# Optimization experiments

Measured on AMD Instinct MI355X. Metric: run time of the kernel, lower is better.

The kernel has to match this reference:

```python
import jax, jax.numpy as jnp
import numpy as np
import math

B, D, NH, HD, FF, P, IMG = 4, 768, 12, 64, 3072, 16, 256
L = (IMG // P) ** 2      # 256 tokens
PD = P * P * 3           # 768 patch dim
GRID = IMG // P          # 16


def setup_inputs() -> dict:
    key = jax.random.key(0)
    ks = iter(jax.random.split(key, 80))
    def nrm(shape, s=0.02):
        return jax.random.normal(next(ks), shape, jnp.float32) * s
    return {
        "x": jax.random.normal(next(ks), (B, 3, IMG, IMG), jnp.float32),
        "pe_norm_w": jnp.ones((PD,), jnp.float32),
        "pe_proj_w": nrm((PD, D)),
        "pe_proj_b": jnp.zeros((D,), jnp.float32),
        "pe_norm_out_w": jnp.ones((D,), jnp.float32),
        "pos_embed": nrm((1, L, D)),
        "in_attn_norm_w": jnp.ones((6, D), jnp.float32),
        "in_qkv_w": nrm((6, D, 3 * D)),
        "in_out_w": nrm((6, D, D)),
        "in_ff_norm_w": jnp.ones((6, D), jnp.float32),
        "in_w1": nrm((6, D, 2 * FF)),
        "in_w2": nrm((6, FF, D)),
        "mid_attn_norm_w": jnp.ones((3, D), jnp.float32),
        "mid_qkv_w": nrm((3, D, 3 * D)),
        "mid_out_w": nrm((3, D, D)),
        "mid_ff_norm_w": jnp.ones((3, D), jnp.float32),
        "mid_w1": nrm((3, D, 2 * FF)),
        "mid_w2": nrm((3, FF, D)),
        "out_skip_w": nrm((2 * D, D)),
        "out_skip_b": jnp.zeros((D,), jnp.float32),
        "out_attn_norm_w": jnp.ones((D,), jnp.float32),
        "out_qkv_w": nrm((D, 3 * D)),
        "out_out_w": nrm((D, D)),
        "out_ff_norm_w": jnp.ones((D,), jnp.float32),
        "out_w1": nrm((D, 2 * FF)),
        "out_w2": nrm((FF, D)),
        "final_norm_w": jnp.ones((D,), jnp.float32),
        "ol_proj_w": nrm((D, PD)),
        "ol_proj_b": jnp.zeros((PD,), jnp.float32),
        "rb_conv_in_w": nrm((128, 3, 3, 3), 0.1),
        "rb_gn_w": jnp.ones((5, 128), jnp.float32),
        "rb_gn_b": jnp.zeros((5, 128), jnp.float32),
        "rb_conv1_w": nrm((128, 1, 5, 5), 0.1),
        "rb_conv2_w": nrm((128, 1, 5, 5), 0.1),
        "head_conv_w": nrm((1, 128, 3, 3), 0.1),
    }


def _mish(x):
    return x * jnp.tanh(jax.nn.softplus(x))


def _rms(x, w, eps=1e-5):
    return x * jax.lax.rsqrt(jnp.mean(x * x, axis=-1, keepdims=True) + eps) * w


def _attn(x, qkv_w, out_w):
    b, l, _ = x.shape
    q, k, v = jnp.split(x @ qkv_w, 3, axis=-1)
    s = 1.0 / math.sqrt(HD)  # applied to BOTH q and k, as in source
    q = (q * s).reshape(b, l, NH, HD)
    k = (k * s).reshape(b, l, NH, HD)
    v = v.reshape(b, l, NH, HD)
    logits = jnp.einsum('bqhd,bkhd->bhqk', q, k).astype(jnp.float32)
    w = jax.nn.softmax(logits, axis=-1).astype(x.dtype)
    o = jnp.einsum('bhqk,bkhd->bqhd', w, v).reshape(b, l, NH * HD)
    return o @ out_w


def _ff(x, w1, w2):
    a, g = jnp.split(x @ w1, 2, axis=-1)
    return (_mish(a) * g) @ w2


def _block(x, an, qkv, ow, fn, w1, w2):
    x = x + _attn(_rms(x, an), qkv, ow)
    x = x + _ff(_rms(x, fn), w1, w2)
    return x


def _gn(x, w, b, groups=8, eps=1e-5):
    bb, c, h, ww = x.shape
    xg = x.reshape(bb, groups, c // groups, h, ww)
    m = jnp.mean(xg, axis=(2, 3, 4), keepdims=True)
    v = jnp.var(xg, axis=(2, 3, 4), keepdims=True)
    xn = ((xg - m) * jax.lax.rsqrt(v + eps)).reshape(bb, c, h, ww)
    return xn * w[:, None, None] + b[:, None, None]


def _conv(x, w, pad, dil=1, groups=1):
    xp = jnp.pad(x, ((0, 0), (0, 0), (pad, pad), (pad, pad)), mode='reflect')
    return jax.lax.conv_general_dilated(
        xp, w, window_strides=(1, 1), padding='VALID', rhs_dilation=(dil, dil),
        feature_group_count=groups, dimension_numbers=('NCHW', 'OIHW', 'NCHW'))


def _forward(x, pe_norm_w, pe_proj_w, pe_proj_b, pe_norm_out_w, pos_embed,
             in_attn_norm_w, in_qkv_w, in_out_w, in_ff_norm_w, in_w1, in_w2,
             mid_attn_norm_w, mid_qkv_w, mid_out_w, mid_ff_norm_w, mid_w1, mid_w2,
             out_skip_w, out_skip_b, out_attn_norm_w, out_qkv_w, out_out_w,
             out_ff_norm_w, out_w1, out_w2, final_norm_w, ol_proj_w, ol_proj_b,
             rb_conv_in_w, rb_gn_w, rb_gn_b, rb_conv1_w, rb_conv2_w, head_conv_w):
    b = x.shape[0]
    # PatchEmbed: b c (h p1) (w p2) -> b (h w) (p1 p2 c)
    t = x.reshape(b, 3, GRID, P, GRID, P).transpose(0, 2, 4, 3, 5, 1).reshape(b, L, PD)
    t = _rms(t, pe_norm_w)
    t = t @ pe_proj_w + pe_proj_b
    t = _rms(t, pe_norm_out_w)
    t = t + pos_embed
    # U-ViT trunk: 6 in blocks (skips saved), 3 middle, 1 out block (source typo -> single out block)
    skips = []
    for i in range(6):
        t = _block(t, in_attn_norm_w[i], in_qkv_w[i], in_out_w[i],
                   in_ff_norm_w[i], in_w1[i], in_w2[i])
        skips.append(t)
    for i in range(3):
        t = _block(t, mid_attn_norm_w[i], mid_qkv_w[i], mid_out_w[i],
                   mid_ff_norm_w[i], mid_w1[i], mid_w2[i])
    t = jnp.concatenate([t, skips[-1]], axis=-1) @ out_skip_w + out_skip_b
    t = _block(t, out_attn_norm_w, out_qkv_w, out_out_w, out_ff_norm_w, out_w1, out_w2)
    t = _rms(t, final_norm_w)
    # OutBlock: proj, dropout(eval=identity), unpatchify to b 3 256 256
    t = t @ ol_proj_w + ol_proj_b
    img = t.reshape(b, GRID, GRID, P, P, 3).transpose(0, 5, 1, 3, 2, 4).reshape(b, 3, IMG, IMG)
    # ResNetBlock(128)
    h = _conv(img, rb_conv_in_w, 1)
    h = _mish(_gn(h, rb_gn_w[0], rb_gn_b[0]))
    res = h
    h = _mish(_gn(_conv(h, rb_conv1_w, 2, 1, 128), rb_gn_w[1], rb_gn_b[1]))
    h = res + h
    h = _mish(_gn(h, rb_gn_w[2], rb_gn_b[2]))
    res = h
    h = _mish(_gn(_conv(h, rb_conv2_w, 6, 3, 128), rb_gn_w[3], rb_gn_b[3]))
    h = res + h
    h = _mish(_gn(h, rb_gn_w[4], rb_gn_b[4]))
    return _conv(h, head_conv_w, 1)  # [B, 1, 256, 256]


def reference(x, pe_norm_w, pe_proj_w, pe_proj_b, pe_norm_out_w, pos_embed,
              in_attn_norm_w, in_qkv_w, in_out_w, in_ff_norm_w, in_w1, in_w2,
              mid_attn_norm_w, mid_qkv_w, mid_out_w, mid_ff_norm_w, mid_w1, mid_w2,
              out_skip_w, out_skip_b, out_attn_norm_w, out_qkv_w, out_out_w,
              out_ff_norm_w, out_w1, out_w2, final_norm_w, ol_proj_w, ol_proj_b,
              rb_conv_in_w, rb_gn_w, rb_gn_b, rb_conv1_w, rb_conv2_w, head_conv_w):
    return _forward(x, pe_norm_w, pe_proj_w, pe_proj_b, pe_norm_out_w, pos_embed,
                    in_attn_norm_w, in_qkv_w, in_out_w, in_ff_norm_w, in_w1, in_w2,
                    mid_attn_norm_w, mid_qkv_w, mid_out_w, mid_ff_norm_w, mid_w1, mid_w2,
                    out_skip_w, out_skip_b, out_attn_norm_w, out_qkv_w, out_out_w,
                    out_ff_norm_w, out_w1, out_w2, final_norm_w, ol_proj_w, ol_proj_b,
                    rb_conv_in_w, rb_gn_w, rb_gn_b, rb_conv1_w, rb_conv2_w, head_conv_w)
```

## Files before the change

### kernel.cpp

```cpp
#include <hip/hip_runtime.h>
#include <math.h>

#define B_ 4
#define D_ 768
#define NH_ 12
#define HD_ 64
#define FF_ 3072
#define L_ 256
#define PD_ 768
#define GRID_ 16
#define P_ 16
#define IMG_ 256
#define M_ (B_*L_)
#define NCONV_ (B_*128*IMG_*IMG_)

typedef __attribute__((ext_vector_type(8))) short short8;
typedef __attribute__((ext_vector_type(4))) float f32x4;
typedef __attribute__((ext_vector_type(4))) unsigned short us4;
typedef __attribute__((ext_vector_type(8))) unsigned short us8;
typedef unsigned short ushort_t;

__device__ __forceinline__ float mishf(float x){
    float e = __expf(x);
    float u = (1.f + e) * (1.f + e);
    return x * (1.f - 2.f / (u + 1.f));
}

__device__ __forceinline__ int refl(int i, int n){
    if (i < 0) i = -i;
    if (i >= n) i = 2*n - 2 - i;
    return i;
}

__device__ __forceinline__ ushort_t f2bf(float f){
    unsigned int u = __float_as_uint(f);
    unsigned int r = (u + 0x7FFFu + ((u >> 16) & 1u)) >> 16;
    return (ushort_t)r;
}
__device__ __forceinline__ float bf2f(ushort_t u){
    return __uint_as_float(((unsigned int)u) << 16);
}

__device__ __forceinline__ void block_red2(float& s, float& q){
    #pragma unroll
    for (int o = 32; o > 0; o >>= 1){ s += __shfl_down(s, o); q += __shfl_down(q, o); }
    __shared__ float r1[4], r2[4];
    int tid = threadIdx.x;
    if ((tid & 63) == 0){ r1[tid>>6] = s; r2[tid>>6] = q; }
    __syncthreads();
    if (tid == 0){ s = r1[0]+r1[1]+r1[2]+r1[3]; q = r2[0]+r2[1]+r2[2]+r2[3]; }
    __syncthreads();
}

__global__ __launch_bounds__(256) void k_patchify(const float* __restrict__ x, float* __restrict__ t){
    int idx = blockIdx.x*256 + threadIdx.x;
    int d = idx % PD_; int l = (idx/PD_) % L_; int b = idx/(PD_*L_);
    int c = d % 3; int p = d / 3; int p1 = p / P_; int p2 = p % P_;
    int gh = l / GRID_; int gw = l % GRID_;
    int sy = gh*P_ + p1, sx = gw*P_ + p2;
    t[idx] = x[(((size_t)b*3 + c)*IMG_ + sy)*IMG_ + sx];
}

__global__ __launch_bounds__(256) void k_wt(const float* __restrict__ b0, const float* __restrict__ b1,
                                            const float* __restrict__ b2, int n0, int n1,
                                            ushort_t* __restrict__ dst, int K, int N){
    int z = blockIdx.z;
    size_t sz = (size_t)K * N;
    const float* src = (z < n0) ? b0 + (size_t)z*sz
                     : (z < n0+n1) ? b1 + (size_t)(z-n0)*sz
                     : b2 + (size_t)(z-n0-n1)*sz;
    ushort_t* out = dst + (size_t)z*sz;
    __shared__ float ld[32][33];
    int k0 = blockIdx.y*32, nc0 = blockIdx.x*32;
    int tid = threadIdx.x;
    int c = tid & 31, r8 = tid >> 5;
    #pragma unroll
    for (int i = 0; i < 4; ++i){
        int k = r8 + i*8;
        ld[k][c] = src[(size_t)(k0+k)*N + nc0 + c];
    }
    __syncthreads();
    #pragma unroll
    for (int i = 0; i < 4; ++i){
        int n = r8 + i*8;
        out[(size_t)(nc0+n)*K + k0 + c] = f2bf(ld[c][n]);
    }
}

template<bool OUT_BF>
__global__ __launch_bounds__(256) void k_rms(const float* __restrict__ x, const float* __restrict__ w,
                                             const float* __restrict__ addv, void* __restrict__ yv){
    int row = blockIdx.x;
    const float* xr = x + (size_t)row * D_;
    float s = 0.f;
    for (int i = threadIdx.x; i < D_; i += 256){ float v = xr[i]; s += v*v; }
    __shared__ float red[256];
    red[threadIdx.x] = s; __syncthreads();
    for (int o = 128; o > 0; o >>= 1){
        if (threadIdx.x < o) red[threadIdx.x] += red[threadIdx.x+o];
        __syncthreads();
    }
    float rstd = rsqrtf(red[0]/(float)D_ + 1e-5f);
    int l = row % L_;
    for (int i = threadIdx.x; i < D_; i += 256){
        float v = xr[i]*rstd*w[i];
        if (addv) v += addv[(size_t)l*D_ + i];
        if (OUT_BF) ((ushort_t*)yv)[(size_t)row*D_ + i] = f2bf(v);
        else        ((float*)yv)[(size_t)row*D_ + i] = v;
    }
}

template<bool OBF, int SPLITK>
__global__ __launch_bounds__(256) void k_gemm(const ushort_t* __restrict__ A, const ushort_t* __restrict__ Wt,
                                              void* __restrict__ Cv, const float* __restrict__ bias,
                                              const float* __restrict__ res, int N, int K){
    __shared__ ushort_t As[2][64][40];
    __shared__ ushort_t Ws[2][64][40];
    int tid = threadIdx.x;
    int lane = tid & 63, wid = tid >> 6;
    int wr = wid >> 1, wc = wid & 1;
    int row0 = blockIdx.y * 64, col0 = blockIdx.x * 64;
    f32x4 acc[2][2];
    #pragma unroll
    for (int i = 0; i < 2; ++i)
        #pragma unroll
        for (int j = 0; j < 2; ++j) acc[i][j] = (f32x4){0.f,0.f,0.f,0.f};

    int lg = lane >> 4, lr = lane & 15;
    int sr = tid >> 2, sk = (tid & 3) * 8;
    int kc = K / SPLITK;
    int k0 = (SPLITK > 1) ? blockIdx.z * kc : 0;
    const ushort_t* arow = A  + (size_t)(row0 + sr)*K + k0 + sk;
    const ushort_t* wrow = Wt + (size_t)(col0 + sr)*K + k0 + sk;

    for (int kt = 0; kt < kc; kt += 64){
        __syncthreads();
        *(short8*)&As[0][sr][sk] = *(const short8*)(arow + kt);
        *(short8*)&As[1][sr][sk] = *(const short8*)(arow + kt + 32);
        *(short8*)&Ws[0][sr][sk] = *(const short8*)(wrow + kt);
        *(short8*)&Ws[1][sr][sk] = *(const short8*)(wrow + kt + 32);
        __syncthreads();
        short8 a0[2], a1[2], b0[2], b1[2];
        #pragma unroll
        for (int i = 0; i < 2; ++i){
            a0[i] = *(const short8*)(&As[0][wr*32 + i*16 + lr][lg*8]);
            a1[i] = *(const short8*)(&As[1][wr*32 + i*16 + lr][lg*8]);
        }
        #pragma unroll
        for (int j = 0; j < 2; ++j){
            b0[j] = *(const short8*)(&Ws[0][wc*32 + j*16 + lr][lg*8]);
            b1[j] = *(const short8*)(&Ws[1][wc*32 + j*16 + lr][lg*8]);
        }
        #pragma unroll
        for (int i = 0; i < 2; ++i)
            #pragma unroll
            for (int j = 0; j < 2; ++j){
                acc[i][j] = __builtin_amdgcn_mfma_f32_16x16x32_bf16(a0[i], b0[j], acc[i][j], 0, 0, 0);
                acc[i][j] = __builtin_amdgcn_mfma_f32_16x16x32_bf16(a1[i], b1[j], acc[i][j], 0, 0, 0);
            }
    }
    if (SPLITK > 1){
        float* Pp = (float*)Cv + (size_t)blockIdx.z * M_ * N;
        #pragma unroll
        for (int i = 0; i < 2; ++i)
            #pragma unroll
            for (int j = 0; j < 2; ++j)
                #pragma unroll
                for (int q = 0; q < 4; ++q){
                    int m = row0 + wr*32 + i*16 + lg*4 + q;
                    int n = col0 + wc*32 + j*16 + lr;
                    Pp[(size_t)m*N + n] = acc[i][j][q];
                }
    } else {
        #pragma unroll
        for (int i = 0; i < 2; ++i)
            #pragma unroll
            for (int j = 0; j < 2; ++j)
                #pragma unroll
                for (int q = 0; q < 4; ++q){
                    int m = row0 + wr*32 + i*16 + lg*4 + q;
                    int n = col0 + wc*32 + j*16 + lr;
                    float v = acc[i][j][q];
                    if (bias) v += bias[n];
                    size_t o = (size_t)m*N + n;
                    if (OBF){
                        ((ushort_t*)Cv)[o] = f2bf(v);
                    } else {
                        if (res) v += res[o];
                        ((float*)Cv)[o] = v;
                    }
                }
    }
}

__global__ __launch_bounds__(256) void k_skred(const float* __restrict__ Pp, float* __restrict__ t){
    int idx = blockIdx.x*256 + threadIdx.x;
    size_t e = (size_t)idx*4;
    f32x4 s = *(const f32x4*)(t + e);
    #pragma unroll
    for (int z = 0; z < 4; ++z){
        f32x4 v = *(const f32x4*)(Pp + (size_t)z*M_*D_ + e);
        s.x += v.x; s.y += v.y; s.z += v.z; s.w += v.w;
    }
    *(f32x4*)(t + e) = s;
}

__global__ __launch_bounds__(256) void k_gemm_glu(const ushort_t* __restrict__ A, const ushort_t* __restrict__ Wt,
                                                  ushort_t* __restrict__ Cb, int K){
    __shared__ ushort_t As[2][64][40];
    __shared__ ushort_t Wa[2][64][40];
    __shared__ ushort_t Wg[2][64][40];
    int tid = threadIdx.x;
    int lane = tid & 63, wid = tid >> 6;
    int wr = wid >> 1, wc = wid & 1;
    int row0 = blockIdx.y * 64, col0 = blockIdx.x * 64;
    f32x4 aa[2][2], ag[2][2];
    #pragma unroll
    for (int i = 0; i < 2; ++i)
        #pragma unroll
        for (int j = 0; j < 2; ++j){ aa[i][j] = (f32x4){0.f,0.f,0.f,0.f}; ag[i][j] = (f32x4){0.f,0.f,0.f,0.f}; }

    int lg = lane >> 4, lr = lane & 15;
    int sr = tid >> 2, sk = (tid & 3) * 8;
    const ushort_t* arow = A + (size_t)(row0+sr)*K + sk;
    const ushort_t* war = Wt + (size_t)(col0+sr)*K + sk;
    const ushort_t* wgr = Wt + (size_t)(FF_+col0+sr)*K + sk;

    for (int kt = 0; kt < K; kt += 64){
        __syncthreads();
        *(short8*)&As[0][sr][sk] = *(const short8*)(arow + kt);
        *(short8*)&As[1][sr][sk] = *(const short8*)(arow + kt + 32);
        *(short8*)&Wa[0][sr][sk] = *(const short8*)(war + kt);
        *(short8*)&Wa[1][sr][sk] = *(const short8*)(war + kt + 32);
        *(short8*)&Wg[0][sr][sk] = *(const short8*)(wgr + kt);
        *(short8*)&Wg[1][sr][sk] = *(const short8*)(wgr + kt + 32);
        __syncthreads();
        short8 a0[2], a1[2], ba0[2], ba1[2], bg0[2], bg1[2];
        #pragma unroll
        for (int i = 0; i < 2; ++i){
            a0[i] = *(const short8*)(&As[0][wr*32 + i*16 + lr][lg*8]);
            a1[i] = *(const short8*)(&As[1][wr*32 + i*16 + lr][lg*8]);
        }
        #pragma unroll
        for (int j = 0; j < 2; ++j){
            ba0[j] = *(const short8*)(&Wa[0][wc*32 + j*16 + lr][lg*8]);
            ba1[j] = *(const short8*)(&Wa[1][wc*32 + j*16 + lr][lg*8]);
            bg0[j] = *(const short8*)(&Wg[0][wc*32 + j*16 + lr][lg*8]);
            bg1[j] = *(const short8*)(&Wg[1][wc*32 + j*16 + lr][lg*8]);
        }
        #pragma unroll
        for (int i = 0; i < 2; ++i)
            #pragma unroll
            for (int j = 0; j < 2; ++j){
                aa[i][j] = __builtin_amdgcn_mfma_f32_16x16x32_bf16(a0[i], ba0[j], aa[i][j], 0, 0, 0);
                aa[i][j] = __builtin_amdgcn_mfma_f32_16x16x32_bf16(a1[i], ba1[j], aa[i][j], 0, 0, 0);
                ag[i][j] = __builtin_amdgcn_mfma_f32_16x16x32_bf16(a0[i], bg0[j], ag[i][j], 0, 0, 0);
                ag[i][j] = __builtin_amdgcn_mfma_f32_16x16x32_bf16(a1[i], bg1[j], ag[i][j], 0, 0, 0);
            }
    }
    #pragma unroll
    for (int i = 0; i < 2; ++i)
        #pragma unroll
        for (int j = 0; j < 2; ++j)
            #pragma unroll
            for (int q = 0; q < 4; ++q){
                int m = row0 + wr*32 + i*16 + lg*4 + q;
                int n = col0 + wc*32 + j*16 + lr;
                Cb[(size_t)m*FF_ + n] = f2bf(mishf(aa[i][j][q]) * ag[i][j][q]);
            }
}

__global__ __launch_bounds__(256) void k_attn(const ushort_t* __restrict__ qkv, ushort_t* __restrict__ out){
    int qt = blockIdx.x, h = blockIdx.y, b = blockIdx.z;
    const ushort_t* base = qkv + (size_t)b * L_ * 3 * D_;
    __shared__ ushort_t Qs[64][72];
    __shared__ ushort_t KVs[64][72];
    __shared__ ushort_t Ps[64][268];
    __shared__ float red[8][64];
    int tid = threadIdx.x;
    int lane = tid & 63, w = tid >> 6;
    int lr = lane & 15, lg = lane >> 4;

    {
        int r = tid >> 2, c = (tid & 3) * 16;
        const ushort_t* src = base + (size_t)(qt*64 + r)*3*D_ + h*HD_ + c;
        *(us8*)&Qs[r][c]   = *(const us8*)src;
        *(us8*)&Qs[r][c+8] = *(const us8*)(src + 8);
    }

    f32x4 sacc[4][4];
    #pragma unroll
    for (int kt = 0; kt < 4; ++kt)
        #pragma unroll
        for (int mi = 0; mi < 4; ++mi) sacc[kt][mi] = (f32x4){0.f,0.f,0.f,0.f};

    for (int kt = 0; kt < 4; ++kt){
        __syncthreads();
        {
            int r = tid >> 2, c = (tid & 3) * 16;
            const ushort_t* src = base + (size_t)(kt*64 + r)*3*D_ + D_ + h*HD_ + c;
            *(us8*)&KVs[r][c]   = *(const us8*)src;
            *(us8*)&KVs[r][c+8] = *(const us8*)(src + 8);
        }
        __syncthreads();
        short8 bk0 = *(const short8*)&KVs[w*16 + lr][lg*8];
        short8 bk1 = *(const short8*)&KVs[w*16 + lr][32 + lg*8];
        #pragma unroll
        for (int mi = 0; mi < 4; ++mi){
            short8 a0 = *(const short8*)&Qs[mi*16 + lr][lg*8];
            short8 a1 = *(const short8*)&Qs[mi*16 + lr][32 + lg*8];
            sacc[kt][mi] = __builtin_amdgcn_mfma_f32_16x16x32_bf16(a0, bk0, sacc[kt][mi], 0, 0, 0);
            sacc[kt][mi] = __builtin_amdgcn_mfma_f32_16x16x32_bf16(a1, bk1, sacc[kt][mi], 0, 0, 0);
        }
    }

    const float inv64 = 1.0f/64.0f;
    float gm[4][4], linv[4][4];
    #pragma unroll
    for (int mi = 0; mi < 4; ++mi){
        #pragma unroll
        for (int r = 0; r < 4; ++r){
            float v = fmaxf(fmaxf(sacc[0][mi][r], sacc[1][mi][r]), fmaxf(sacc[2][mi][r], sacc[3][mi][r]));
            v = fmaxf(v, __shfl_xor(v, 1));
            v = fmaxf(v, __shfl_xor(v, 2));
            v = fmaxf(v, __shfl_xor(v, 4));
            v = fmaxf(v, __shfl_xor(v, 8));
            gm[mi][r] = v;
            if (lr == 0) red[w][mi*16 + lg*4 + r] = v;
        }
    }
    __syncthreads();
    #pragma unroll
    for (int mi = 0; mi < 4; ++mi){
        #pragma unroll
        for (int r = 0; r < 4; ++r){
            int row = mi*16 + lg*4 + r;
            float m = fmaxf(fmaxf(red[0][row], red[1][row]), fmaxf(red[2][row], red[3][row]));
            gm[mi][r] = m;
            float sum = 0.f;
            #pragma unroll
            for (int kt = 0; kt < 4; ++kt){
                float p = __expf((sacc[kt][mi][r] - m) * inv64);
                Ps[row][kt*64 + w*16 + lr] = f2bf(p);
                sum += p;
            }
            sum += __shfl_xor(sum, 1);
            sum += __shfl_xor(sum, 2);
            sum += __shfl_xor(sum, 4);
            sum += __shfl_xor(sum, 8);
            linv[mi][r] = sum;
            if (lr == 0) red[4 + w][row] = sum;
        }
    }
    __syncthreads();
    #pragma unroll
    for (int mi = 0; mi < 4; ++mi){
        #pragma unroll
        for (int r = 0; r < 4; ++r){
            int row = mi*16 + lg*4 + r;
            linv[mi][r] = 1.0f / (red[4][row] + red[5][row] + red[6][row] + red[7][row]);
        }
    }

    f32x4 oacc[4];
    #pragma unroll
    for (int mi = 0; mi < 4; ++mi) oacc[mi] = (f32x4){0.f,0.f,0.f,0.f};
    for (int kt = 0; kt < 4; ++kt){
        __syncthreads();
        {
            int k = tid & 63, dg = tid >> 6;
            const ushort_t* src = base + (size_t)(kt*64 + k)*3*D_ + 2*D_ + h*HD_ + dg*16;
            us8 v0 = *(const us8*)src;
            us8 v1 = *(const us8*)(src + 8);
            #pragma unroll
            for (int j = 0; j < 8; ++j) KVs[dg*16 + j][k] = v0[j];
            #pragma unroll
            for (int j = 0; j < 8; ++j) KVs[dg*16 + 8 + j][k] = v1[j];
        }
        __syncthreads();
        short8 bv0 = *(const short8*)&KVs[w*16 + lr][lg*8];
        short8 bv1 = *(const short8*)&KVs[w*16 + lr][32 + lg*8];
        #pragma unroll
        for (int mi = 0; mi < 4; ++mi){
            short8 a0 = *(const short8*)&Ps[mi*16 + lr][kt*64 + lg*8];
            short8 a1 = *(const short8*)&Ps[mi*16 + lr][kt*64 + 32 + lg*8];
            oacc[mi] = __builtin_amdgcn_mfma_f32_16x16x32_bf16(a0, bv0, oacc[mi], 0, 0, 0);
            oacc[mi] = __builtin_amdgcn_mfma_f32_16x16x32_bf16(a1, bv1, oacc[mi], 0, 0, 0);
        }
    }
    #pragma unroll
    for (int mi = 0; mi < 4; ++mi){
        #pragma unroll
        for (int r = 0; r < 4; ++r){
            int row = mi*16 + lg*4 + r;
            out[((size_t)(b*L_ + qt*64 + row))*D_ + h*HD_ + w*16 + lr] = f2bf(oacc[mi][r] * linv[mi][r]);
        }
    }
}

__global__ __launch_bounds__(256) void k_cat(const float* __restrict__ t, const float* __restrict__ skip,
                                             ushort_t* __restrict__ cat){
    int i4 = (blockIdx.x*256 + threadIdx.x) * 4;
    int r = i4 / D_, c = i4 % D_;
    float4 a = *(const float4*)(t + i4);
    float4 b = *(const float4*)(skip + i4);
    us4 ua, ub;
    ua.x=f2bf(a.x); ua.y=f2bf(a.y); ua.z=f2bf(a.z); ua.w=f2bf(a.w);
    ub.x=f2bf(b.x); ub.y=f2bf(b.y); ub.z=f2bf(b.z); ub.w=f2bf(b.w);
    *(us4*)(cat + (size_t)r*1536 + c) = ua;
    *(us4*)(cat + (size_t)r*1536 + 768 + c) = ub;
}

__global__ __launch_bounds__(256) void k_unpatchify(const float* __restrict__ t, float* __restrict__ img){
    int idx = blockIdx.x*256 + threadIdx.x;
    int sx = idx % IMG_; int sy = (idx/IMG_)%IMG_; int c = (idx/(IMG_*IMG_))%3; int b = idx/(3*IMG_*IMG_);
    int gh = sy / P_, p1 = sy % P_, gw = sx / P_, p2 = sx % P_;
    img[idx] = t[(((size_t)b*L_) + gh*GRID_+gw)*PD_ + (p1*P_+p2)*3 + c];
}

__global__ __launch_bounds__(256) void k_conv_in(const float* __restrict__ img, const float* __restrict__ w,
                                                 ushort_t* __restrict__ out, float* __restrict__ partial){
    int y = blockIdx.x, b = blockIdx.y;
    int x = threadIdx.x;
    __shared__ float rows[9][IMG_];
    int yy0 = refl(y-1, IMG_), yy2 = refl(y+1, IMG_);
    #pragma unroll
    for (int ic = 0; ic < 3; ++ic){
        const float* basep = img + ((size_t)(b*3+ic))*IMG_*IMG_;
        rows[ic*3+0][x] = basep[(size_t)yy0*IMG_ + x];
        rows[ic*3+1][x] = basep[(size_t)y  *IMG_ + x];
        rows[ic*3+2][x] = basep[(size_t)yy2*IMG_ + x];
    }
    __syncthreads();
    int xl = (x==0)?1:x-1, xr = (x==255)?254:x+1;
    float sg = 0.f, qg = 0.f;
    for (int oc = 0; oc < 128; ++oc){
        const float* wv = w + oc*27;
        float acc = 0.f;
        #pragma unroll
        for (int ic = 0; ic < 3; ++ic){
            const float* wk = wv + ic*9;
            acc += rows[ic*3+0][xl]*wk[0] + rows[ic*3+0][x]*wk[1] + rows[ic*3+0][xr]*wk[2]
                 + rows[ic*3+1][xl]*wk[3] + rows[ic*3+1][x]*wk[4] + rows[ic*3+1][xr]*wk[5]
                 + rows[ic*3+2][xl]*wk[6] + rows[ic*3+2][x]*wk[7] + rows[ic*3+2][xr]*wk[8];
        }
        out[(((size_t)(b*128+oc))*IMG_ + y)*IMG_ + x] = f2bf(acc);
        sg += acc; qg += acc*acc;
        if ((oc & 15) == 15){
            block_red2(sg, qg);
            if (threadIdx.x == 0){
                int pidx = ((b*8 + (oc>>4))*256 + y);
                partial[pidx*2] = sg; partial[pidx*2+1] = qg;
            }
            sg = 0.f; qg = 0.f;
        }
    }
}

__global__ __launch_bounds__(256) void k_gn_fin(const float* __restrict__ partial, int nper,
                                                float* __restrict__ stats){
    int bg = blockIdx.x, tid = threadIdx.x;
    float s = 0.f, q = 0.f;
    for (int i = tid; i < nper; i += 256){
        s += partial[((size_t)bg*nper + i)*2];
        q += partial[((size_t)bg*nper + i)*2 + 1];
    }
    block_red2(s, q);
    if (tid == 0){
        const float n = 16.f*IMG_*IMG_;
        float m = s/n;
        float var = q/n - m*m;
        stats[bg*2]   = m;
        stats[bg*2+1] = rsqrtf(var + 1e-5f);
    }
}

__global__ __launch_bounds__(256) void k_act(const ushort_t* __restrict__ x, const float* __restrict__ st,
                                             const float* __restrict__ gw, const float* __restrict__ gb,
                                             ushort_t* __restrict__ y){
    int bid = blockIdx.x;
    int b = bid >> 11, c = (bid >> 4) & 127;
    int bg = b*8 + (c>>4);
    float sc = st[bg*2+1]*gw[c], sb = gb[c] - st[bg*2]*sc;
    size_t e0 = (size_t)bid*4096 + threadIdx.x*16;
    us8 v0 = *(const us8*)(x + e0), v1 = *(const us8*)(x + e0 + 8);
    us8 r0, r1;
    #pragma unroll
    for (int i = 0; i < 8; ++i) r0[i] = f2bf(mishf(bf2f(v0[i])*sc + sb));
    #pragma unroll
    for (int i = 0; i < 8; ++i) r1[i] = f2bf(mishf(bf2f(v1[i])*sc + sb));
    *(us8*)(y + e0) = r0;
    *(us8*)(y + e0 + 8) = r1;
}

template<int PAD, int DIL>
__global__ __launch_bounds__(256) void k_dw(const ushort_t* __restrict__ in,
                                            const float* __restrict__ cw,
                                            ushort_t* __restrict__ out, float* __restrict__ partial){
    constexpr int AP = (DIL==1) ? 4 : 8;
    constexpr int SC = (DIL==1) ? 44 : 52;
    constexpr int SY = 64 + 2*PAD;
    constexpr int CH = SC/4;
    __shared__ float tile[SY*SC];
    int tileid = blockIdx.x, c = blockIdx.y, b = blockIdx.z;
    int x0 = (tileid & 7) * 32, y0 = (tileid >> 3) * 64;
    int tid = threadIdx.x;
    const ushort_t* ip = in + ((size_t)(b*128+c))*IMG_*IMG_;
    int xs = x0 - AP;
    if (xs >= 0 && xs + SC <= IMG_){
        for (int j = tid; j < SY*CH; j += 256){
            int r = j / CH, q = j - r*CH;
            int gy = refl(y0 - PAD + r, IMG_);
            us4 v = *(const us4*)(ip + (size_t)gy*IMG_ + xs + q*4);
            f32x4 fv = { bf2f(v.x), bf2f(v.y), bf2f(v.z), bf2f(v.w) };
            *(f32x4*)&tile[r*SC + q*4] = fv;
        }
    } else {
        for (int j = tid; j < SY*SC; j += 256){
            int r = j / SC, cc = j - r*SC;
            int gy = refl(y0 - PAD + r, IMG_);
            int gx = refl(xs + cc, IMG_);
            tile[r*SC + cc] = bf2f(ip[(size_t)gy*IMG_ + gx]);
        }
    }
    __syncthreads();
    float wreg[25];
    #pragma unroll
    for (int u = 0; u < 25; ++u) wreg[u] = cw[c*25 + u];
    int tx4 = (tid & 7)*4, ty = tid >> 3;
    constexpr int NV = (DIL==1) ? 3 : 5;
    float s = 0.f, q2 = 0.f;
    #pragma unroll
    for (int rr = 0; rr < 2; ++rr){
        int yy = ty + rr*32;
        float acc[4] = {0.f,0.f,0.f,0.f};
        #pragma unroll
        for (int kh = 0; kh < 5; ++kh){
            const float* rowp = &tile[(yy + kh*DIL)*SC + tx4];
            float vv[NV*4];
            #pragma unroll
            for (int u = 0; u < NV; ++u){
                f32x4 v = *(const f32x4*)(rowp + u*4);
                vv[u*4]=v.x; vv[u*4+1]=v.y; vv[u*4+2]=v.z; vv[u*4+3]=v.w;
            }
            #pragma unroll
            for (int kw = 0; kw < 5; ++kw){
                float wk = wreg[kh*5+kw];
                #pragma unroll
                for (int j = 0; j < 4; ++j)
                    acc[j] += vv[kw*DIL + j + (AP - 2*DIL)] * wk;
            }
        }
        us4 o4 = { f2bf(acc[0]), f2bf(acc[1]), f2bf(acc[2]), f2bf(acc[3]) };
        *(us4*)(out + (((size_t)(b*128+c))*IMG_ + y0+yy)*IMG_ + x0+tx4) = o4;
        s  += acc[0]+acc[1]+acc[2]+acc[3];
        q2 += acc[0]*acc[0]+acc[1]*acc[1]+acc[2]*acc[2]+acc[3]*acc[3];
    }
    block_red2(s, q2);
    if (tid == 0){
        int bid = (b*128 + c)*32 + tileid;
        partial[bid*2] = s; partial[bid*2+1] = q2;
    }
}

__global__ __launch_bounds__(256) void k_addmish(const ushort_t* __restrict__ xn, const float* __restrict__ stn,
                                                 const float* __restrict__ wn, const float* __restrict__ bn,
                                                 const ushort_t* __restrict__ resa,
                                                 ushort_t* __restrict__ out, float* __restrict__ partial){
    int bid = blockIdx.x;
    int b = bid >> 11, c = (bid >> 4) & 127;
    int bg = b*8 + (c>>4);
    float scn = stn[bg*2+1]*wn[c], sbn = bn[c] - stn[bg*2]*scn;
    size_t e0 = (size_t)bid*4096 + threadIdx.x*16;
    us8 vn0 = *(const us8*)(xn + e0), vn1 = *(const us8*)(xn + e0 + 8);
    us8 vr0 = *(const us8*)(resa + e0), vr1 = *(const us8*)(resa + e0 + 8);
    us8 r0, r1;
    float s = 0.f, q = 0.f;
    #pragma unroll
    for (int i = 0; i < 8; ++i){
        float v = mishf(bf2f(vn0[i])*scn + sbn) + bf2f(vr0[i]);
        s += v; q += v*v; r0[i] = f2bf(v);
    }
    #pragma unroll
    for (int i = 0; i < 8; ++i){
        float v = mishf(bf2f(vn1[i])*scn + sbn) + bf2f(vr1[i]);
        s += v; q += v*v; r1[i] = f2bf(v);
    }
    *(us8*)(out + e0) = r0;
    *(us8*)(out + e0 + 8) = r1;
    block_red2(s, q);
    if (threadIdx.x == 0){ partial[bid*2] = s; partial[bid*2+1] = q; }
}

__global__ __launch_bounds__(256) void k_head_part(const ushort_t* __restrict__ in, const float* __restrict__ st,
                                                   const float* __restrict__ gw, const float* __restrict__ gb,
                                                   const float* __restrict__ w, float* __restrict__ part){
    __shared__ float tile[34*34];
    int tileid = blockIdx.x, cg = blockIdx.y, b = blockIdx.z;
    int x0 = (tileid & 7)*32, y0 = (tileid >> 3)*32;
    int tid = threadIdx.x;
    int tx4 = (tid & 7)*4, ty = tid >> 3;
    float m  = st[(b*8+cg)*2];
    float rs = st[(b*8+cg)*2 + 1];
    float acc[4] = {0.f,0.f,0.f,0.f};
    for (int ci = 0; ci < 16; ++ci){
        int c = cg*16 + ci;
        float sc = rs*gw[c], sb = gb[c] - m*sc;
        const ushort_t* ip = in + ((size_t)(b*128+c))*IMG_*IMG_;
        if (ci) __syncthreads();
        for (int i = tid; i < 34*34; i += 256){
            int r = i/34, cc = i - r*34;
            int gy = refl(y0-1+r, IMG_);
            int gx = refl(x0-1+cc, IMG_);
            tile[i] = mishf(bf2f(ip[(size_t)gy*IMG_+gx])*sc + sb);
        }
        __syncthreads();
        const float* wc = w + c*9;
        #pragma unroll
        for (int kh = 0; kh < 3; ++kh){
            float vv[6];
            #pragma unroll
            for (int u = 0; u < 6; ++u) vv[u] = tile[(ty+kh)*34 + tx4 + u];
            #pragma unroll
            for (int kw = 0; kw < 3; ++kw){
                float wk = wc[kh*3+kw];
                #pragma unroll
                for (int j = 0; j < 4; ++j) acc[j] += vv[kw+j]*wk;
            }
        }
    }
    f32x4 o = {acc[0], acc[1], acc[2], acc[3]};
    *(f32x4*)(part + (((size_t)(cg*4+b))*IMG_ + y0+ty)*IMG_ + x0+tx4) = o;
}

__global__ __launch_bounds__(256) void k_head_fin(const float* __restrict__ part, float* __restrict__ out){
    int idx4 = blockIdx.x*256 + threadIdx.x;
    size_t e = (size_t)idx4*4;
    int b = (int)(e / (IMG_*IMG_));
    size_t off = e % (IMG_*IMG_);
    f32x4 s = {0.f,0.f,0.f,0.f};
    #pragma unroll
    for (int cg = 0; cg < 8; ++cg){
        f32x4 v = *(const f32x4*)(part + (size_t)(cg*4+b)*IMG_*IMG_ + off);
        s.x += v.x; s.y += v.y; s.z += v.z; s.w += v.w;
    }
    *(f32x4*)(out + e) = s;
}


struct WsMap {
    float *t, *skip, *t2, *ybuf, *img, *partial, *hpart, *stats, *part;
    ushort_t *nb, *qkvb, *ab, *gbuf, *cat, *wb_qkv, *wb_out, *wb_w1, *wb_w2, *wb_pe, *wb_skip, *wb_ol, *cA, *cB;
};

static void run_block(const float* an, const ushort_t* qw, const ushort_t* ow,
                      const float* fn, const ushort_t* w1, const ushort_t* w2,
                      float* t, const WsMap& W, hipStream_t stream){
    k_rms<true><<<M_, 256, 0, stream>>>(t, an, nullptr, W.nb);
    k_gemm<true,1><<<dim3(3*D_/64, M_/64), 256, 0, stream>>>(W.nb, qw, W.qkvb, nullptr, nullptr, 3*D_, D_);
    k_attn<<<dim3(4, NH_, B_), 256, 0, stream>>>(W.qkvb, W.ab);
    k_gemm<false,1><<<dim3(D_/64, M_/64), 256, 0, stream>>>(W.ab, ow, t, nullptr, t, D_, D_);
    k_rms<true><<<M_, 256, 0, stream>>>(t, fn, nullptr, W.nb);
    k_gemm_glu<<<dim3(FF_/64, M_/64), 256, 0, stream>>>(W.nb, w1, W.gbuf, D_);
    k_gemm<false,4><<<dim3(D_/64, M_/64, 4), 256, 0, stream>>>(W.gbuf, w2, W.part, nullptr, nullptr, D_, FF_);
    k_skred<<<(M_*D_)/1024, 256, 0, stream>>>(W.part, t);
}

extern "C" void kernel_launch(void* const* d_in, const int* in_sizes, int n_in,
                              void* d_out, int out_size, void* d_ws, size_t ws_size,
                              hipStream_t stream){
    const float* x              = (const float*)d_in[0];
    const float* pe_norm_w      = (const float*)d_in[1];
    const float* pe_proj_w      = (const float*)d_in[2];
    const float* pe_proj_b      = (const float*)d_in[3];
    const float* pe_norm_out_w  = (const float*)d_in[4];
    const float* pos_embed      = (const float*)d_in[5];
    const float* in_attn_norm_w = (const float*)d_in[6];
    const float* in_qkv_w       = (const float*)d_in[7];
    const float* in_out_w       = (const float*)d_in[8];
    const float* in_ff_norm_w   = (const float*)d_in[9];
    const float* in_w1          = (const float*)d_in[10];
    const float* in_w2          = (const float*)d_in[11];
    const float* mid_attn_norm_w= (const float*)d_in[12];
    const float* mid_qkv_w      = (const float*)d_in[13];
    const float* mid_out_w      = (const float*)d_in[14];
    const float* mid_ff_norm_w  = (const float*)d_in[15];
    const float* mid_w1         = (const float*)d_in[16];
    const float* mid_w2         = (const float*)d_in[17];
    const float* out_skip_w     = (const float*)d_in[18];
    const float* out_skip_b     = (const float*)d_in[19];
    const float* out_attn_norm_w= (const float*)d_in[20];
    const float* out_qkv_w      = (const float*)d_in[21];
    const float* out_out_w      = (const float*)d_in[22];
    const float* out_ff_norm_w  = (const float*)d_in[23];
    const float* out_w1         = (const float*)d_in[24];
    const float* out_w2         = (const float*)d_in[25];
    const float* final_norm_w   = (const float*)d_in[26];
    const float* ol_proj_w      = (const float*)d_in[27];
    const float* ol_proj_b      = (const float*)d_in[28];
    const float* rb_conv_in_w   = (const float*)d_in[29];
    const float* rb_gn_w        = (const float*)d_in[30];
    const float* rb_gn_b        = (const float*)d_in[31];
    const float* rb_conv1_w     = (const float*)d_in[32];
    const float* rb_conv2_w     = (const float*)d_in[33];
    const float* head_conv_w    = (const float*)d_in[34];

    WsMap W;
    float* f = (float*)d_ws;
    const size_t TD = (size_t)M_*D_;
    W.t      = f;               f += TD;
    W.skip   = f;               f += TD;
    W.t2     = f;               f += TD;
    W.ybuf   = f;               f += TD;
    W.img    = f;               f += TD;
    W.partial= f;               f += 131072;
    W.hpart  = f;               f += (size_t)8*4*IMG_*IMG_;
    W.stats  = f;               f += 448;
    W.part   = f;               f += (size_t)4*TD;
    ushort_t* u = (ushort_t*)f;
    W.nb     = u;               u += TD;
    W.qkvb   = u;               u += (size_t)M_*3*D_;
    W.ab     = u;               u += TD;
    W.gbuf   = u;               u += (size_t)M_*FF_;
    W.cat    = u;               u += (size_t)M_*2*D_;
    W.wb_qkv = u;               u += (size_t)10*D_*3*D_;
    W.wb_out = u;               u += (size_t)10*D_*D_;
    W.wb_w1  = u;               u += (size_t)10*D_*2*FF_;
    W.wb_w2  = u;               u += (size_t)10*FF_*D_;
    W.wb_pe  = u;               u += (size_t)D_*D_;
    W.wb_skip= u;               u += (size_t)2*D_*D_;
    W.wb_ol  = u;               u += (size_t)D_*D_;
    W.cA     = u;               u += (size_t)NCONV_;
    W.cB     = u;

    float* st0 = W.stats;       float* st1 = W.stats + 64;
    float* st2 = W.stats + 128; float* st3 = W.stats + 192;
    float* st4 = W.stats + 256;

    k_wt<<<dim3(3*D_/32, D_/32, 10), 256, 0, stream>>>(in_qkv_w, mid_qkv_w, out_qkv_w, 6, 3, W.wb_qkv, D_, 3*D_);
    k_wt<<<dim3(D_/32, D_/32, 10), 256, 0, stream>>>(in_out_w, mid_out_w, out_out_w, 6, 3, W.wb_out, D_, D_);
    k_wt<<<dim3(2*FF_/32, D_/32, 10), 256, 0, stream>>>(in_w1, mid_w1, out_w1, 6, 3, W.wb_w1, D_, 2*FF_);
    k_wt<<<dim3(D_/32, FF_/32, 10), 256, 0, stream>>>(in_w2, mid_w2, out_w2, 6, 3, W.wb_w2, FF_, D_);
    k_wt<<<dim3(D_/32, D_/32, 1), 256, 0, stream>>>(pe_proj_w, nullptr, nullptr, 1, 0, W.wb_pe, D_, D_);
    k_wt<<<dim3(D_/32, 2*D_/32, 1), 256, 0, stream>>>(out_skip_w, nullptr, nullptr, 1, 0, W.wb_skip, 2*D_, D_);
    k_wt<<<dim3(D_/32, D_/32, 1), 256, 0, stream>>>(ol_proj_w, nullptr, nullptr, 1, 0, W.wb_ol, D_, D_);

    k_patchify<<<(B_*L_*PD_)/256, 256, 0, stream>>>(x, W.t2);
    k_rms<true><<<M_, 256, 0, stream>>>(W.t2, pe_norm_w, nullptr, W.nb);
    k_gemm<false,1><<<dim3(D_/64, M_/64), 256, 0, stream>>>(W.nb, W.wb_pe, W.t, pe_proj_b, nullptr, D_, D_);
    k_rms<false><<<M_, 256, 0, stream>>>(W.t, pe_norm_out_w, pos_embed, W.t);

    for (int i = 0; i < 6; ++i){
        run_block(in_attn_norm_w + (size_t)i*D_, W.wb_qkv + (size_t)i*D_*3*D_,
                  W.wb_out + (size_t)i*D_*D_, in_ff_norm_w + (size_t)i*D_,
                  W.wb_w1 + (size_t)i*D_*2*FF_, W.wb_w2 + (size_t)i*FF_*D_,
                  W.t, W, stream);
    }
    hipMemcpyAsync(W.skip, W.t, TD*sizeof(float), hipMemcpyDeviceToDevice, stream);

    for (int i = 0; i < 3; ++i){
        int z = 6 + i;
        run_block(mid_attn_norm_w + (size_t)i*D_, W.wb_qkv + (size_t)z*D_*3*D_,
                  W.wb_out + (size_t)z*D_*D_, mid_ff_norm_w + (size_t)i*D_,
                  W.wb_w1 + (size_t)z*D_*2*FF_, W.wb_w2 + (size_t)z*FF_*D_,
                  W.t, W, stream);
    }

    k_cat<<<(M_*D_)/1024, 256, 0, stream>>>(W.t, W.skip, W.cat);
    k_gemm<false,1><<<dim3(D_/64, M_/64), 256, 0, stream>>>(W.cat, W.wb_skip, W.t2, out_skip_b, nullptr, D_, 2*D_);

    run_block(out_attn_norm_w, W.wb_qkv + (size_t)9*D_*3*D_, W.wb_out + (size_t)9*D_*D_,
              out_ff_norm_w, W.wb_w1 + (size_t)9*D_*2*FF_, W.wb_w2 + (size_t)9*FF_*D_,
              W.t2, W, stream);

    k_rms<true><<<M_, 256, 0, stream>>>(W.t2, final_norm_w, nullptr, W.nb);
    k_gemm<false,1><<<dim3(PD_/64, M_/64), 256, 0, stream>>>(W.nb, W.wb_ol, W.ybuf, ol_proj_b, nullptr, PD_, D_);
    k_unpatchify<<<(B_*3*IMG_*IMG_)/256, 256, 0, stream>>>(W.ybuf, W.img);

    k_conv_in<<<dim3(256, 4), 256, 0, stream>>>(W.img, rb_conv_in_w, W.cA, W.partial);
    k_gn_fin<<<32, 256, 0, stream>>>(W.partial, 256, st0);
    k_act<<<8192, 256, 0, stream>>>(W.cA, st0, rb_gn_w, rb_gn_b, W.cB);
    k_dw<2,1><<<dim3(32, 128, 4), 256, 0, stream>>>(W.cB, rb_conv1_w, W.cA, W.partial);
    k_gn_fin<<<32, 256, 0, stream>>>(W.partial, 512, st1);
    k_addmish<<<8192, 256, 0, stream>>>(W.cA, st1, rb_gn_w+128, rb_gn_b+128, W.cB, W.cA, W.partial);
    k_gn_fin<<<32, 256, 0, stream>>>(W.partial, 256, st2);
    k_act<<<8192, 256, 0, stream>>>(W.cA, st2, rb_gn_w+256, rb_gn_b+256, W.cB);
    k_dw<6,3><<<dim3(32, 128, 4), 256, 0, stream>>>(W.cB, rb_conv2_w, W.cA, W.partial);
    k_gn_fin<<<32, 256, 0, stream>>>(W.partial, 512, st3);
    k_addmish<<<8192, 256, 0, stream>>>(W.cA, st3, rb_gn_w+384, rb_gn_b+384, W.cB, W.cA, W.partial);
    k_gn_fin<<<32, 256, 0, stream>>>(W.partial, 256, st4);
    k_head_part<<<dim3(64, 8, 4), 256, 0, stream>>>(W.cA, st4, rb_gn_w+512, rb_gn_b+512, head_conv_w, W.hpart);
    k_head_fin<<<(B_*IMG_*IMG_)/1024, 256, 0, stream>>>(W.hpart, (float*)d_out);
}
```

Baseline: 1.533 ms.

## Fuse split-K reduction with next RMSNorm, halve split-K, parallelize conv_in channels

The FF2 split-K reduction now runs in a per-row kernel that also computes the following block's attention RMSNorm and writes its bf16 input. This removes one separate norm launch and one pass over the activations per block. Split-K for FF2 drops from 4 to 2, so there is less partial traffic but fewer blocks in that GEMM. conv_in is split across four output-channel groups to raise parallelism, at the cost of re-reading the input rows in each group. The depthwise conv's shared tile stride is also reduced.

```diff
diff --git a/kernel.cpp b/kernel.cpp
--- a/kernel.cpp
+++ b/kernel.cpp
@@ -107,6 +107,36 @@
         if (addv) v += addv[(size_t)l*D_ + i];
         if (OUT_BF) ((ushort_t*)yv)[(size_t)row*D_ + i] = f2bf(v);
         else        ((float*)yv)[(size_t)row*D_ + i] = v;
+    }
+}
+
+__global__ __launch_bounds__(256) void k_skred_rms(const float* __restrict__ Pp, float* __restrict__ t,
+                                                   const float* __restrict__ w, ushort_t* __restrict__ nb){
+    int row = blockIdx.x;
+    int tid = threadIdx.x;
+    float v[3];
+    float s = 0.f;
+    #pragma unroll
+    for (int i = 0; i < 3; ++i){
+        int c = tid + i*256;
+        size_t o = (size_t)row*D_ + c;
+        float x = t[o] + Pp[o] + Pp[(size_t)M_*D_ + o];
+        v[i] = x; s += x*x;
+        t[o] = x;
+    }
+    #pragma unroll
+    for (int o = 32; o > 0; o >>= 1) s += __shfl_down(s, o);
+    __shared__ float r1[4];
+    if ((tid & 63) == 0) r1[tid>>6] = s;
+    __syncthreads();
+    float tot = r1[0]+r1[1]+r1[2]+r1[3];
+    float rstd = rsqrtf(tot*(1.f/768.f) + 1e-5f);
+    if (w){
+        #pragma unroll
+        for (int i = 0; i < 3; ++i){
+            int c = tid + i*256;
+            nb[(size_t)row*D_ + c] = f2bf(v[i]*rstd*w[c]);
+        }
     }
 }
 
@@ -193,18 +223,6 @@
     }
 }
 
-__global__ __launch_bounds__(256) void k_skred(const float* __restrict__ Pp, float* __restrict__ t){
-    int idx = blockIdx.x*256 + threadIdx.x;
-    size_t e = (size_t)idx*4;
-    f32x4 s = *(const f32x4*)(t + e);
-    #pragma unroll
-    for (int z = 0; z < 4; ++z){
-        f32x4 v = *(const f32x4*)(Pp + (size_t)z*M_*D_ + e);
-        s.x += v.x; s.y += v.y; s.z += v.z; s.w += v.w;
-    }
-    *(f32x4*)(t + e) = s;
-}
-
 __global__ __launch_bounds__(256) void k_gemm_glu(const ushort_t* __restrict__ A, const ushort_t* __restrict__ Wt,
                                                   ushort_t* __restrict__ Cb, int K){
     __shared__ ushort_t As[2][64][40];
@@ -420,7 +438,7 @@
 
 __global__ __launch_bounds__(256) void k_conv_in(const float* __restrict__ img, const float* __restrict__ w,
                                                  ushort_t* __restrict__ out, float* __restrict__ partial){
-    int y = blockIdx.x, b = blockIdx.y;
+    int y = blockIdx.x, ocg = blockIdx.y, b = blockIdx.z;
     int x = threadIdx.x;
     __shared__ float rows[9][IMG_];
     int yy0 = refl(y-1, IMG_), yy2 = refl(y+1, IMG_);
@@ -434,7 +452,7 @@
     __syncthreads();
     int xl = (x==0)?1:x-1, xr = (x==255)?254:x+1;
     float sg = 0.f, qg = 0.f;
-    for (int oc = 0; oc < 128; ++oc){
+    for (int oc = ocg*32; oc < ocg*32 + 32; ++oc){
         const float* wv = w + oc*27;
         float acc = 0.f;
         #pragma unroll
@@ -498,7 +516,7 @@
                                             const float* __restrict__ cw,
                                             ushort_t* __restrict__ out, float* __restrict__ partial){
     constexpr int AP = (DIL==1) ? 4 : 8;
-    constexpr int SC = (DIL==1) ? 44 : 52;
+    constexpr int SC = (DIL==1) ? 40 : 48;
     constexpr int SY = 64 + 2*PAD;
     constexpr int CH = SC/4;
     __shared__ float tile[SY*SC];
@@ -653,17 +671,16 @@
     ushort_t *nb, *qkvb, *ab, *gbuf, *cat, *wb_qkv, *wb_out, *wb_w1, *wb_w2, *wb_pe, *wb_skip, *wb_ol, *cA, *cB;
 };
 
-static void run_block(const float* an, const ushort_t* qw, const ushort_t* ow,
-                      const float* fn, const ushort_t* w1, const ushort_t* w2,
+static void run_block(const float* fn, const ushort_t* qw, const ushort_t* ow,
+                      const ushort_t* w1, const ushort_t* w2, const float* next_w,
                       float* t, const WsMap& W, hipStream_t stream){
-    k_rms<true><<<M_, 256, 0, stream>>>(t, an, nullptr, W.nb);
     k_gemm<true,1><<<dim3(3*D_/64, M_/64), 256, 0, stream>>>(W.nb, qw, W.qkvb, nullptr, nullptr, 3*D_, D_);
     k_attn<<<dim3(4, NH_, B_), 256, 0, stream>>>(W.qkvb, W.ab);
     k_gemm<false,1><<<dim3(D_/64, M_/64), 256, 0, stream>>>(W.ab, ow, t, nullptr, t, D_, D_);
     k_rms<true><<<M_, 256, 0, stream>>>(t, fn, nullptr, W.nb);
     k_gemm_glu<<<dim3(FF_/64, M_/64), 256, 0, stream>>>(W.nb, w1, W.gbuf, D_);
-    k_gemm<false,4><<<dim3(D_/64, M_/64, 4), 256, 0, stream>>>(W.gbuf, w2, W.part, nullptr, nullptr, D_, FF_);
-    k_skred<<<(M_*D_)/1024, 256, 0, stream>>>(W.part, t);
+    k_gemm<false,2><<<dim3(D_/64, M_/64, 2), 256, 0, stream>>>(W.gbuf, w2, W.part, nullptr, nullptr, D_, FF_);
+    k_skred_rms<<<M_, 256, 0, stream>>>(W.part, t, next_w, W.nb);
 }
 
 extern "C" void kernel_launch(void* const* d_in, const int* in_sizes, int n_in,
@@ -749,35 +766,38 @@
     k_rms<true><<<M_, 256, 0, stream>>>(W.t2, pe_norm_w, nullptr, W.nb);
     k_gemm<false,1><<<dim3(D_/64, M_/64), 256, 0, stream>>>(W.nb, W.wb_pe, W.t, pe_proj_b, nullptr, D_, D_);
     k_rms<false><<<M_, 256, 0, stream>>>(W.t, pe_norm_out_w, pos_embed, W.t);
+    k_rms<true><<<M_, 256, 0, stream>>>(W.t, in_attn_norm_w, nullptr, W.nb);
 
     for (int i = 0; i < 6; ++i){
-        run_block(in_attn_norm_w + (size_t)i*D_, W.wb_qkv + (size_t)i*D_*3*D_,
-                  W.wb_out + (size_t)i*D_*D_, in_ff_norm_w + (size_t)i*D_,
+        const float* next_w = (i < 5) ? in_attn_norm_w + (size_t)(i+1)*D_ : mid_attn_norm_w;
+        run_block(in_ff_norm_w + (size_t)i*D_, W.wb_qkv + (size_t)i*D_*3*D_,
+                  W.wb_out + (size_t)i*D_*D_,
                   W.wb_w1 + (size_t)i*D_*2*FF_, W.wb_w2 + (size_t)i*FF_*D_,
-                  W.t, W, stream);
+                  next_w, W.t, W, stream);
     }
     hipMemcpyAsync(W.skip, W.t, TD*sizeof(float), hipMemcpyDeviceToDevice, stream);
 
     for (int i = 0; i < 3; ++i){
         int z = 6 + i;
-        run_block(mid_attn_norm_w + (size_t)i*D_, W.wb_qkv + (size_t)z*D_*3*D_,
-                  W.wb_out + (size_t)z*D_*D_, mid_ff_norm_w + (size_t)i*D_,
+        const float* next_w = (i < 2) ? mid_attn_norm_w + (size_t)(i+1)*D_ : nullptr;
+        run_block(mid_ff_norm_w + (size_t)i*D_, W.wb_qkv + (size_t)z*D_*3*D_,
+                  W.wb_out + (size_t)z*D_*D_,
                   W.wb_w1 + (size_t)z*D_*2*FF_, W.wb_w2 + (size_t)z*FF_*D_,
-                  W.t, W, stream);
+                  next_w, W.t, W, stream);
     }
 
     k_cat<<<(M_*D_)/1024, 256, 0, stream>>>(W.t, W.skip, W.cat);
     k_gemm<false,1><<<dim3(D_/64, M_/64), 256, 0, stream>>>(W.cat, W.wb_skip, W.t2, out_skip_b, nullptr, D_, 2*D_);
 
-    run_block(out_attn_norm_w, W.wb_qkv + (size_t)9*D_*3*D_, W.wb_out + (size_t)9*D_*D_,
-              out_ff_norm_w, W.wb_w1 + (size_t)9*D_*2*FF_, W.wb_w2 + (size_t)9*FF_*D_,
-              W.t2, W, stream);
-
-    k_rms<true><<<M_, 256, 0, stream>>>(W.t2, final_norm_w, nullptr, W.nb);
+    k_rms<true><<<M_, 256, 0, stream>>>(W.t2, out_attn_norm_w, nullptr, W.nb);
+    run_block(out_ff_norm_w, W.wb_qkv + (size_t)9*D_*3*D_, W.wb_out + (size_t)9*D_*D_,
+              W.wb_w1 + (size_t)9*D_*2*FF_, W.wb_w2 + (size_t)9*FF_*D_,
+              final_norm_w, W.t2, W, stream);
+
     k_gemm<false,1><<<dim3(PD_/64, M_/64), 256, 0, stream>>>(W.nb, W.wb_ol, W.ybuf, ol_proj_b, nullptr, PD_, D_);
     k_unpatchify<<<(B_*3*IMG_*IMG_)/256, 256, 0, stream>>>(W.ybuf, W.img);
 
-    k_conv_in<<<dim3(256, 4), 256, 0, stream>>>(W.img, rb_conv_in_w, W.cA, W.partial);
+    k_conv_in<<<dim3(256, 4, 4), 256, 0, stream>>>(W.img, rb_conv_in_w, W.cA, W.partial);
     k_gn_fin<<<32, 256, 0, stream>>>(W.partial, 256, st0);
     k_act<<<8192, 256, 0, stream>>>(W.cA, st0, rb_gn_w, rb_gn_b, W.cB);
     k_dw<2,1><<<dim3(32, 128, 4), 256, 0, stream>>>(W.cB, rb_conv1_w, W.cA, W.partial);
```

Result: no change. 1.522 ms (-0.8%).
